# Optimization experiments

Hardware: AMD Instinct MI355X
Metric: run time of the kernel (lower is better)

## Reference

```python
import jax, jax.numpy as jnp
import numpy as np

B = 131072
K = 1024
D = 16 * 8  # hard-coded feature dim in the torch module


def setup_inputs() -> dict:
    key = jax.random.key(0)
    kx, kw = jax.random.split(key)
    x = jax.random.normal(kx, (B, D), dtype=jnp.float32)
    # xavier_normal_ init: std = sqrt(2 / (fan_in + fan_out)) = sqrt(2 / (K + D))
    std = np.sqrt(2.0 / (K + D)).astype(np.float32)
    cluster_weights = jax.random.normal(kw, (K, D), dtype=jnp.float32) * std
    return {"x": x, "cluster_weights": cluster_weights}


def reference(x, cluster_weights):
    bn = x.shape[0]
    k = cluster_weights.shape[0]
    x = x.reshape(bn, -1)  # [B, D]
    # (same math as the original broadcasted (x - w)^2 sum, without the [B,K,D] blow-up)
    x2 = jnp.sum(x * x, axis=1, keepdims=True)               # [B, 1]
    w2 = jnp.sum(cluster_weights * cluster_weights, axis=1)  # [K]
    d = x2 + w2[None, :] - 2.0 * jnp.matmul(x, cluster_weights.T)  # [B, K]
    cl = jnp.argmin(d, axis=1)  # [B] int
    # distance to assigned centroid, summed
    inertia_loss = jnp.sum(jnp.take_along_axis(d, cl[:, None], axis=1))
    # xe_loss = sum_{i,j} (1 if i==j else -1) * <w_i, w_j>
    #         = 2 * trace(W W^T) - sum(W W^T)
    G = jnp.matmul(cluster_weights, cluster_weights.T)  # [K, K]
    xe_loss = 2.0 * jnp.trace(G) - jnp.sum(G)
    return inertia_loss / bn, xe_loss / k, cl
```

## Files before the change

### kernel.cpp

```cpp
#include <hip/hip_runtime.h>
#include <float.h>
#include <limits.h>
#include <math.h>


#define TAU 1e-3f

using bf16x8 = __attribute__((ext_vector_type(8))) short;
using f32x4  = __attribute__((ext_vector_type(4))) float;
using s16x4  = __attribute__((ext_vector_type(4))) short;

static __device__ __forceinline__ short f2bf_trunc(float f) {
    return (short)(__float_as_uint(f) >> 16);
}
static __device__ __forceinline__ float bf2f(short h) {
    return __uint_as_float(((unsigned int)(unsigned short)h) << 16);
}
static __device__ __forceinline__ bool lexlt(float v1, int i1, float v2, int i2) {
    return v1 < v2 || (v1 == v2 && i1 < i2);
}
static __device__ __forceinline__ void gload_lds16(const void* g, void* l) {
    __builtin_amdgcn_global_load_lds(
        (const __attribute__((address_space(1))) unsigned int*)g,
        (__attribute__((address_space(3))) unsigned int*)l, 16, 0, 0);
}
#define FENCE() do { asm volatile("" ::: "memory"); __builtin_amdgcn_sched_barrier(0); } while (0)

__global__ void wprep_kernel(const float* __restrict__ W, float* __restrict__ w2,
                             short* __restrict__ whl, int write_whl)
{
    const int k = blockIdx.x;
    const int d = threadIdx.x;
    float v = W[(size_t)k * 128 + d];
    float sq = v * v;
    for (int off = 1; off < 64; off <<= 1) sq += __shfl_xor(sq, off, 64);
    __shared__ float p[2];
    if ((d & 63) == 0) p[d >> 6] = sq;
    __syncthreads();
    if (d == 0) w2[k] = p[0] + p[1];
    if (write_whl) {
        short h = f2bf_trunc(v);
        short l = f2bf_trunc(v - bf2f(h));
        const int tile = k >> 7, c = k & 127;
        size_t base = (size_t)tile * 32768 + (size_t)(c >> 4) * 2048 + (size_t)(d >> 5) * 512
                    + (size_t)((d >> 3) & 3) * 128 + (size_t)(c & 15) * 8 + (size_t)(d & 7);
        whl[base]         = h;
        whl[base + 16384] = l;
    }
}

__global__ __launch_bounds__(512, 1)
void dist_argmin_mfma(const float* __restrict__ X, const short* __restrict__ whl,
                      const float* __restrict__ w2g, float* __restrict__ cl_out,
                      double* __restrict__ inertia_acc,
                      int* __restrict__ flag_cnt, int* __restrict__ flag_rows,
                      int flag_cap)
{
    __shared__ __align__(16) char smem[137856];
    char*   lB0  = smem;
    char*   lB1  = smem + 65536;
    float*  lw2  = (float*)(smem + 131072);
    float*  lx2  = (float*)(smem + 135168);
    int*    mscr = (int*)(smem + 135680);
    double* dred = (double*)(smem + 137728);

    const int tid    = threadIdx.x;
    const int lane   = tid & 63;
    const int laneLo = lane & 15;
    const int laneHi = lane >> 4;
    const int wid    = tid >> 6;
    const int rowg   = wid >> 1;
    const int colg   = wid & 1;
    const int rowbase = blockIdx.x * 128;

    lw2[tid]       = w2g[tid];
    lw2[tid + 512] = w2g[tid + 512];

    {
        const int r = tid >> 2, q = tid & 3;
        float s = 0.f;
        short* Areg = (short*)lB0;
        #pragma unroll
        for (int j = 0; j < 8; ++j) {
            const int d0 = q * 4 + j * 16;
            float4 v = *reinterpret_cast<const float4*>(X + (size_t)(rowbase + r) * 128 + d0);
            float fv[4] = {v.x, v.y, v.z, v.w};
            s16x4 hv, lv;
            #pragma unroll
            for (int u = 0; u < 4; ++u) {
                s = fmaf(fv[u], fv[u], s);
                short h = f2bf_trunc(fv[u]);
                short l = f2bf_trunc(fv[u] - bf2f(h));
                hv[u] = h; lv[u] = l;
            }
            const int kb = d0 >> 3, off = d0 & 7;
            short* pa = Areg + ((size_t)kb * 128 + r) * 8 + off;
            *reinterpret_cast<s16x4*>(pa)         = hv;
            *reinterpret_cast<s16x4*>(pa + 16384) = lv;
        }
        s += __shfl_xor(s, 1, 64);
        s += __shfl_xor(s, 2, 64);
        if (q == 0) lx2[r] = s;
    }
    __syncthreads();

    bf16x8 ah[2][4], al[2][4];
    {
        const char* pA = lB0 + laneHi * 2048 + (rowg * 32 + laneLo) * 16;
        #pragma unroll
        for (int k0b = 0; k0b < 4; ++k0b)
            #pragma unroll
            for (int m = 0; m < 2; ++m) {
                ah[m][k0b] = *reinterpret_cast<const bf16x8*>(pA + k0b * 8192 + m * 256);
                al[m][k0b] = *reinterpret_cast<const bf16x8*>(pA + 32768 + k0b * 8192 + m * 256);
            }
    }
    asm volatile("s_waitcnt lgkmcnt(0)" ::: "memory");
    __builtin_amdgcn_sched_barrier(0);
    __builtin_amdgcn_s_barrier();
    FENCE();

    #pragma unroll
    for (int q = 0; q < 8; ++q)
        gload_lds16((const char*)whl + (q * 8 + wid) * 1024 + lane * 16,
                    lB0 + (q * 8 + wid) * 1024);

    float t1v[2][4], t2v[2][4];
    int   t1i[2][4];
    #pragma unroll
    for (int m = 0; m < 2; ++m)
        #pragma unroll
        for (int r = 0; r < 4; ++r) {
            t1v[m][r] = FLT_MAX; t2v[m][r] = FLT_MAX; t1i[m][r] = INT_MAX;
        }
    int colv[4];
    #pragma unroll
    for (int nt = 0; nt < 4; ++nt) colv[nt] = colg * 64 + nt * 16 + laneLo;

    const char* pB0 = lB0 + colg * 16384 + lane * 16;
    const char* pB1 = lB1 + colg * 16384 + lane * 16;

    auto compute = [&](int t, const char* pB) {
        float w2v[4];
        #pragma unroll
        for (int nt = 0; nt < 4; ++nt)
            w2v[nt] = lw2[t * 128 + colg * 64 + nt * 16 + laneLo];

        f32x4 acc[2][4];
        #pragma unroll
        for (int m = 0; m < 2; ++m)
            #pragma unroll
            for (int nt = 0; nt < 4; ++nt)
                acc[m][nt] = (f32x4){0.f, 0.f, 0.f, 0.f};

        __builtin_amdgcn_s_setprio(1);
        #pragma unroll
        for (int k0b = 0; k0b < 4; ++k0b) {
            #pragma unroll
            for (int nt = 0; nt < 4; ++nt) {
                bf16x8 bh = *reinterpret_cast<const bf16x8*>(pB + nt * 4096 + k0b * 1024);
                bf16x8 bl = *reinterpret_cast<const bf16x8*>(pB + 32768 + nt * 4096 + k0b * 1024);
                #pragma unroll
                for (int m = 0; m < 2; ++m) {
                    acc[m][nt] = __builtin_amdgcn_mfma_f32_16x16x32_bf16(ah[m][k0b], bh, acc[m][nt], 0, 0, 0);
                    acc[m][nt] = __builtin_amdgcn_mfma_f32_16x16x32_bf16(ah[m][k0b], bl, acc[m][nt], 0, 0, 0);
                    acc[m][nt] = __builtin_amdgcn_mfma_f32_16x16x32_bf16(al[m][k0b], bh, acc[m][nt], 0, 0, 0);
                }
            }
        }
        __builtin_amdgcn_s_setprio(0);

        #pragma unroll
        for (int nt = 0; nt < 4; ++nt)
            #pragma unroll
            for (int m = 0; m < 2; ++m)
                #pragma unroll
                for (int r = 0; r < 4; ++r) {
                    float dv = fmaf(-2.f, acc[m][nt][r], w2v[nt]);
                    float hi = fmaxf(t1v[m][r], dv);
                    t2v[m][r] = fminf(t2v[m][r], hi);
                    bool cnd = dv < t1v[m][r];
                    t1i[m][r] = cnd ? colv[nt] : t1i[m][r];
                    t1v[m][r] = fminf(t1v[m][r], dv);
                }
        #pragma unroll
        for (int nt = 0; nt < 4; ++nt) colv[nt] += 128;
    };

    #pragma unroll 2
    for (int t = 0; t < 7; ++t) {
        char* dst = ((t + 1) & 1) ? lB1 : lB0;
        const char* src = (const char*)whl + (size_t)(t + 1) * 65536;
        #pragma unroll
        for (int q = 0; q < 8; ++q)
            gload_lds16(src + (q * 8 + wid) * 1024 + lane * 16,
                        dst + (q * 8 + wid) * 1024);
        asm volatile("s_waitcnt vmcnt(8)" ::: "memory");
        __builtin_amdgcn_sched_barrier(0);
        __builtin_amdgcn_s_barrier();
        FENCE();
        compute(t, (t & 1) ? pB1 : pB0);
        asm volatile("s_waitcnt lgkmcnt(0)" ::: "memory");
        __builtin_amdgcn_sched_barrier(0);
        __builtin_amdgcn_s_barrier();
        FENCE();
    }
    asm volatile("s_waitcnt vmcnt(0)" ::: "memory");
    __builtin_amdgcn_sched_barrier(0);
    __builtin_amdgcn_s_barrier();
    FENCE();
    compute(7, pB1);

    #pragma unroll
    for (int off = 1; off < 16; off <<= 1) {
        #pragma unroll
        for (int m = 0; m < 2; ++m)
            #pragma unroll
            for (int r = 0; r < 4; ++r) {
                float ov1 = __shfl_xor(t1v[m][r], off, 64);
                int   oi1 = __shfl_xor(t1i[m][r], off, 64);
                float ov2 = __shfl_xor(t2v[m][r], off, 64);
                float nt2 = fminf(fminf(t2v[m][r], ov2), fmaxf(t1v[m][r], ov1));
                if (lexlt(ov1, oi1, t1v[m][r], t1i[m][r])) { t1v[m][r] = ov1; t1i[m][r] = oi1; }
                t2v[m][r] = nt2;
            }
    }

    __syncthreads();
    if (colg == 1 && laneLo == 0) {
        #pragma unroll
        for (int m = 0; m < 2; ++m)
            #pragma unroll
            for (int r = 0; r < 4; ++r) {
                const int row = rowg * 32 + m * 16 + laneHi * 4 + r;
                mscr[row * 4 + 0] = __float_as_int(t1v[m][r]);
                mscr[row * 4 + 1] = t1i[m][r];
                mscr[row * 4 + 2] = __float_as_int(t2v[m][r]);
            }
    }
    __syncthreads();
    double local = 0.0;
    if (colg == 0 && laneLo == 0) {
        #pragma unroll
        for (int m = 0; m < 2; ++m)
            #pragma unroll
            for (int r = 0; r < 4; ++r) {
                const int row = rowg * 32 + m * 16 + laneHi * 4 + r;
                float ov1 = __int_as_float(mscr[row * 4 + 0]);
                int   oi1 = mscr[row * 4 + 1];
                float ov2 = __int_as_float(mscr[row * 4 + 2]);
                float b1v = t1v[m][r], b2v;
                int   b1i = t1i[m][r];
                b2v = fminf(fminf(t2v[m][r], ov2), fmaxf(b1v, ov1));
                if (lexlt(ov1, oi1, b1v, b1i)) { b1v = ov1; b1i = oi1; }
                const int grow = rowbase + row;
                const float gap = b2v - b1v;
                if (gap >= TAU) {
                    cl_out[grow] = (float)b1i;
                    local += (double)(b1v + lx2[row]);
                } else {
                    int slot = atomicAdd(flag_cnt, 1);
                    if (slot < flag_cap) {
                        flag_rows[slot] = grow;
                    } else {
                        cl_out[grow] = (float)b1i;
                        local += (double)(b1v + lx2[row]);
                    }
                }
            }
        dred[rowg * 4 + laneHi] = local;
    }
    __syncthreads();
    if (tid == 0) {
        double tt = 0.0;
        for (int i = 0; i < 16; ++i) tt += dred[i];
        atomicAdd(inertia_acc, tt);
    }
}

__global__ __launch_bounds__(512, 1)
void dist_argmin_v2(const float* __restrict__ X, const float* __restrict__ W,
                    const float* __restrict__ w2g, float* __restrict__ cl_out,
                    double* __restrict__ inertia_acc,
                    int* __restrict__ flag_cnt, int* __restrict__ flag_rows,
                    int flag_cap)
{
    __shared__ __align__(16) char smem[133760];
    short*  Areg = (short*)smem;
    short*  Breg = (short*)(smem + 65536);
    int*    mscr = (int*)(smem + 131072);
    float*  lx2  = (float*)(smem + 131072 + 2048);
    double* dred = (double*)(smem + 131072 + 2048 + 512);

    const int tid    = threadIdx.x;
    const int lane   = tid & 63;
    const int laneLo = lane & 15;
    const int laneHi = lane >> 4;
    const int wid    = tid >> 6;
    const int rowg   = wid >> 1;
    const int colg   = wid & 1;
    const int rowbase = blockIdx.x * 128;

    {
        const int r = tid >> 2, q = tid & 3;
        float s = 0.f;
        #pragma unroll
        for (int j = 0; j < 8; ++j) {
            const int d0 = q * 4 + j * 16;
            float4 v = *reinterpret_cast<const float4*>(X + (size_t)(rowbase + r) * 128 + d0);
            float fv[4] = {v.x, v.y, v.z, v.w};
            s16x4 hv, lv;
            #pragma unroll
            for (int u = 0; u < 4; ++u) {
                s = fmaf(fv[u], fv[u], s);
                short h = f2bf_trunc(fv[u]);
                short l = f2bf_trunc(fv[u] - bf2f(h));
                hv[u] = h; lv[u] = l;
            }
            const int kb = d0 >> 3, off = d0 & 7;
            short* pa = Areg + (kb * 128 + r) * 8 + off;
            *reinterpret_cast<s16x4*>(pa)         = hv;
            *reinterpret_cast<s16x4*>(pa + 16384) = lv;
        }
        s += __shfl_xor(s, 1, 64);
        s += __shfl_xor(s, 2, 64);
        if (q == 0) lx2[r] = s;
    }

    float t1v[2][4], t2v[2][4];
    int   t1i[2][4];
    #pragma unroll
    for (int m = 0; m < 2; ++m)
        #pragma unroll
        for (int r = 0; r < 4; ++r) {
            t1v[m][r] = FLT_MAX; t2v[m][r] = FLT_MAX; t1i[m][r] = INT_MAX;
        }

    const char* pAbase = smem + laneHi * 2048 + (rowg * 32 + laneLo) * 16;
    const char* pBbase = smem + 65536 + colg * 16384 + lane * 16;

    for (int iter = 0; iter < 8; ++iter) {
        __syncthreads();
        {
            const int c = tid >> 2, q = tid & 3;
            const int nt = c >> 4, c15 = c & 15;
            #pragma unroll
            for (int j = 0; j < 8; ++j) {
                const int d0 = q * 4 + j * 16;
                float4 v = *reinterpret_cast<const float4*>(W + (size_t)(iter * 128 + c) * 128 + d0);
                float fv[4] = {v.x, v.y, v.z, v.w};
                s16x4 hv, lv;
                #pragma unroll
                for (int u = 0; u < 4; ++u) {
                    short h = f2bf_trunc(fv[u]);
                    short l = f2bf_trunc(fv[u] - bf2f(h));
                    hv[u] = h; lv[u] = l;
                }
                const int k0b = d0 >> 5, sub = (d0 >> 3) & 3, jj = d0 & 7;
                short* pb = Breg + ((nt * 4 + k0b) * 64 + sub * 16 + c15) * 8 + jj;
                *reinterpret_cast<s16x4*>(pb)         = hv;
                *reinterpret_cast<s16x4*>(pb + 16384) = lv;
            }
        }
        float w2v[4];
        #pragma unroll
        for (int nt = 0; nt < 4; ++nt)
            w2v[nt] = w2g[iter * 128 + colg * 64 + nt * 16 + laneLo];
        __syncthreads();

        f32x4 acc[2][4];
        #pragma unroll
        for (int m = 0; m < 2; ++m)
            #pragma unroll
            for (int nt = 0; nt < 4; ++nt)
                acc[m][nt] = (f32x4){0.f, 0.f, 0.f, 0.f};

        #pragma unroll
        for (int k0b = 0; k0b < 4; ++k0b) {
            bf16x8 ah[2], al[2];
            #pragma unroll
            for (int m = 0; m < 2; ++m) {
                ah[m] = *reinterpret_cast<const bf16x8*>(pAbase + k0b * 8192 + m * 256);
                al[m] = *reinterpret_cast<const bf16x8*>(pAbase + 32768 + k0b * 8192 + m * 256);
            }
            #pragma unroll
            for (int nt = 0; nt < 4; ++nt) {
                bf16x8 bh = *reinterpret_cast<const bf16x8*>(pBbase + nt * 4096 + k0b * 1024);
                bf16x8 bl = *reinterpret_cast<const bf16x8*>(pBbase + 32768 + nt * 4096 + k0b * 1024);
                #pragma unroll
                for (int m = 0; m < 2; ++m) {
                    acc[m][nt] = __builtin_amdgcn_mfma_f32_16x16x32_bf16(ah[m], bh, acc[m][nt], 0, 0, 0);
                    acc[m][nt] = __builtin_amdgcn_mfma_f32_16x16x32_bf16(ah[m], bl, acc[m][nt], 0, 0, 0);
                    acc[m][nt] = __builtin_amdgcn_mfma_f32_16x16x32_bf16(al[m], bh, acc[m][nt], 0, 0, 0);
                }
            }
        }

        #pragma unroll
        for (int nt = 0; nt < 4; ++nt) {
            const int col = iter * 128 + colg * 64 + nt * 16 + laneLo;
            #pragma unroll
            for (int m = 0; m < 2; ++m)
                #pragma unroll
                for (int r = 0; r < 4; ++r) {
                    float dv = fmaf(-2.f, acc[m][nt][r], w2v[nt]);
                    float hi = fmaxf(t1v[m][r], dv);
                    t2v[m][r] = fminf(t2v[m][r], hi);
                    bool cnd = dv < t1v[m][r];
                    t1i[m][r] = cnd ? col : t1i[m][r];
                    t1v[m][r] = fminf(t1v[m][r], dv);
                }
        }
    }

    #pragma unroll
    for (int off = 1; off < 16; off <<= 1) {
        #pragma unroll
        for (int m = 0; m < 2; ++m)
            #pragma unroll
            for (int r = 0; r < 4; ++r) {
                float ov1 = __shfl_xor(t1v[m][r], off, 64);
                int   oi1 = __shfl_xor(t1i[m][r], off, 64);
                float ov2 = __shfl_xor(t2v[m][r], off, 64);
                float nt2 = fminf(fminf(t2v[m][r], ov2), fmaxf(t1v[m][r], ov1));
                if (lexlt(ov1, oi1, t1v[m][r], t1i[m][r])) { t1v[m][r] = ov1; t1i[m][r] = oi1; }
                t2v[m][r] = nt2;
            }
    }

    __syncthreads();
    if (colg == 1 && laneLo == 0) {
        #pragma unroll
        for (int m = 0; m < 2; ++m)
            #pragma unroll
            for (int r = 0; r < 4; ++r) {
                const int row = rowg * 32 + m * 16 + laneHi * 4 + r;
                mscr[row * 4 + 0] = __float_as_int(t1v[m][r]);
                mscr[row * 4 + 1] = t1i[m][r];
                mscr[row * 4 + 2] = __float_as_int(t2v[m][r]);
            }
    }
    __syncthreads();
    double local = 0.0;
    if (colg == 0 && laneLo == 0) {
        #pragma unroll
        for (int m = 0; m < 2; ++m)
            #pragma unroll
            for (int r = 0; r < 4; ++r) {
                const int row = rowg * 32 + m * 16 + laneHi * 4 + r;
                float ov1 = __int_as_float(mscr[row * 4 + 0]);
                int   oi1 = mscr[row * 4 + 1];
                float ov2 = __int_as_float(mscr[row * 4 + 2]);
                float b1v = t1v[m][r], b2v;
                int   b1i = t1i[m][r];
                b2v = fminf(fminf(t2v[m][r], ov2), fmaxf(b1v, ov1));
                if (lexlt(ov1, oi1, b1v, b1i)) { b1v = ov1; b1i = oi1; }
                const int grow = rowbase + row;
                const float gap = b2v - b1v;
                if (gap >= TAU) {
                    cl_out[grow] = (float)b1i;
                    local += (double)(b1v + lx2[row]);
                } else {
                    int slot = atomicAdd(flag_cnt, 1);
                    if (slot < flag_cap) flag_rows[slot] = grow;
                    else { cl_out[grow] = (float)b1i; local += (double)(b1v + lx2[row]); }
                }
            }
        dred[rowg * 4 + laneHi] = local;
    }
    __syncthreads();
    if (tid == 0) {
        double t = 0.0;
        for (int i = 0; i < 16; ++i) t += dred[i];
        atomicAdd(inertia_acc, t);
    }
}

__global__ void refine_kernel(const float* __restrict__ X, const float* __restrict__ W,
                              const int* __restrict__ flag_cnt, const int* __restrict__ flag_rows,
                              int flag_cap, float* __restrict__ cl_out,
                              double* __restrict__ inertia_acc)
{
    __shared__ double sv[4];
    __shared__ int    si[4];
    __shared__ float  xrow[128];
    int n = *flag_cnt;
    if (n > flag_cap) n = flag_cap;
    const int tid = threadIdx.x;

    for (int f = blockIdx.x; f < n; f += gridDim.x) {
        int row = flag_rows[f];
        if (tid < 128) xrow[tid] = X[(size_t)row * 128 + tid];
        __syncthreads();

        double best = DBL_MAX; int bi = INT_MAX;
        for (int cc = 0; cc < 4; ++cc) {
            int c = tid + 256 * cc;
            double dot = 0.0, wsq = 0.0;
            for (int d = 0; d < 128; ++d) {
                double wv = (double)W[(size_t)c * 128 + d];
                dot = fma((double)xrow[d], wv, dot);
                wsq = fma(wv, wv, wsq);
            }
            double dist = wsq - 2.0 * dot;
            if (dist < best || (dist == best && c < bi)) { best = dist; bi = c; }
        }
        for (int off = 1; off < 64; off <<= 1) {
            double ov = __shfl_xor(best, off, 64);
            int    oi = __shfl_xor(bi, off, 64);
            if (ov < best || (ov == best && oi < bi)) { best = ov; bi = oi; }
        }
        if ((tid & 63) == 0) { sv[tid >> 6] = best; si[tid >> 6] = bi; }
        __syncthreads();
        if (tid == 0) {
            for (int wv = 1; wv < 4; ++wv)
                if (sv[wv] < best || (sv[wv] == best && si[wv] < bi)) { best = sv[wv]; bi = si[wv]; }
            double x2 = 0.0;
            for (int d = 0; d < 128; ++d) { double xv = (double)xrow[d]; x2 = fma(xv, xv, x2); }
            cl_out[row] = (float)bi;
            atomicAdd(inertia_acc, x2 + best);
        }
        __syncthreads();
    }
}

__global__ void finalize_kernel(const float* __restrict__ W, const float* __restrict__ w2,
                                const double* __restrict__ inertia, float* __restrict__ out)
{
    __shared__ float sh1[128], sh2[128];
    int d = threadIdx.x;
    float s = 0.f;
    for (int k = 0; k < 1024; ++k) s += W[(size_t)k * 128 + d];
    float t = 0.f;
    for (int j = 0; j < 8; ++j) t += w2[d + 128 * j];
    sh1[d] = s * s;
    sh2[d] = t;
    __syncthreads();
    for (int off = 64; off > 0; off >>= 1) {
        if (d < off) { sh1[d] += sh1[d + off]; sh2[d] += sh2[d + off]; }
        __syncthreads();
    }
    if (d == 0) {
        float xe = 2.f * sh2[0] - sh1[0];
        out[1] = xe / 1024.f;
        out[0] = (float)(*inertia / 131072.0);
    }
}

extern "C" void kernel_launch(void* const* d_in, const int* in_sizes, int n_in,
                              void* d_out, int out_size, void* d_ws, size_t ws_size,
                              hipStream_t stream)
{
    const float* X = (const float*)d_in[0];
    const float* W = (const float*)d_in[1];
    float* out = (float*)d_out;
    char* ws = (char*)d_ws;

    double* inertia  = (double*)ws;
    int*    flag_cnt = (int*)(ws + 8);
    float*  w2       = (float*)(ws + 16);
    short*  whl      = (short*)(ws + 8192);

    const size_t WHL_END = 8192 + 524288;
    const bool precomp = ws_size >= WHL_END + 65536;

    int*   flag_rows;
    int    flag_cap;
    if (precomp) {
        flag_rows = (int*)(ws + WHL_END);
        long cap = ((long)ws_size - (long)WHL_END) / 4;
        flag_cap = cap > 131072 ? 131072 : (int)cap;
    } else {
        flag_rows = (int*)(ws + 8192);
        long cap = ((long)ws_size - 8192) / 4;
        flag_cap = cap < 0 ? 0 : (cap > 131072 ? 131072 : (int)cap);
    }

    hipMemsetAsync(ws, 0, 16, stream);

    wprep_kernel<<<1024, 128, 0, stream>>>(W, w2, whl, precomp ? 1 : 0);
    if (precomp) {
        dist_argmin_mfma<<<1024, 512, 0, stream>>>(X, whl, w2, out + 2, inertia,
                                                   flag_cnt, flag_rows, flag_cap);
    } else {
        dist_argmin_v2<<<1024, 512, 0, stream>>>(X, W, w2, out + 2, inertia,
                                                 flag_cnt, flag_rows, flag_cap);
    }
    refine_kernel<<<1024, 256, 0, stream>>>(X, W, flag_cnt, flag_rows, flag_cap,
                                            out + 2, inertia);
    finalize_kernel<<<1, 128, 0, stream>>>(W, w2, inertia, out);
}
```

Baseline: 202.3 us.

## Halve centroid tile to 64 columns and load X directly into registers

The centroid tile streamed through LDS shrinks from 128 to 64 columns, so the double buffer and shared memory drop to roughly half. Launch bounds now allow several 512-thread blocks per CU. X rows are converted to bf16 hi/lo fragments straight from global memory into registers, which removes the LDS staging pass and one block barrier. The compute loop is reordered per column tile to lower accumulator register pressure, at the cost of more, smaller pipeline iterations and more barriers per block.

```diff
diff --git a/kernel.cpp b/kernel.cpp
--- a/kernel.cpp
+++ b/kernel.cpp
@@ -41,28 +41,28 @@
     if (write_whl) {
         short h = f2bf_trunc(v);
         short l = f2bf_trunc(v - bf2f(h));
-        const int tile = k >> 7, c = k & 127;
-        size_t base = (size_t)tile * 32768 + (size_t)(c >> 4) * 2048 + (size_t)(d >> 5) * 512
+        const int tile = k >> 6, c = k & 63;
+        size_t base = (size_t)tile * 16384 + (size_t)(c >> 4) * 2048 + (size_t)(d >> 5) * 512
                     + (size_t)((d >> 3) & 3) * 128 + (size_t)(c & 15) * 8 + (size_t)(d & 7);
-        whl[base]         = h;
-        whl[base + 16384] = l;
-    }
-}
-
-__global__ __launch_bounds__(512, 1)
+        whl[base]        = h;
+        whl[base + 8192] = l;
+    }
+}
+
+__global__ __launch_bounds__(512, 4)
 void dist_argmin_mfma(const float* __restrict__ X, const short* __restrict__ whl,
                       const float* __restrict__ w2g, float* __restrict__ cl_out,
                       double* __restrict__ inertia_acc,
                       int* __restrict__ flag_cnt, int* __restrict__ flag_rows,
                       int flag_cap)
 {
-    __shared__ __align__(16) char smem[137856];
+    __shared__ __align__(16) char smem[72320];
     char*   lB0  = smem;
-    char*   lB1  = smem + 65536;
-    float*  lw2  = (float*)(smem + 131072);
-    float*  lx2  = (float*)(smem + 135168);
-    int*    mscr = (int*)(smem + 135680);
-    double* dred = (double*)(smem + 137728);
+    char*   lB1  = smem + 32768;
+    float*  lw2  = (float*)(smem + 65536);
+    float*  lx2  = (float*)(smem + 69632);
+    int*    mscr = (int*)(smem + 70144);
+    double* dred = (double*)(smem + 72192);
 
     const int tid    = threadIdx.x;
     const int lane   = tid & 63;
@@ -76,54 +76,39 @@
     lw2[tid]       = w2g[tid];
     lw2[tid + 512] = w2g[tid + 512];
 
-    {
-        const int r = tid >> 2, q = tid & 3;
+    bf16x8 ah[2][4], al[2][4];
+    #pragma unroll
+    for (int m = 0; m < 2; ++m) {
+        const float* xp = X + (size_t)(rowbase + rowg * 32 + m * 16 + laneLo) * 128 + laneHi * 8;
         float s = 0.f;
-        short* Areg = (short*)lB0;
-        #pragma unroll
-        for (int j = 0; j < 8; ++j) {
-            const int d0 = q * 4 + j * 16;
-            float4 v = *reinterpret_cast<const float4*>(X + (size_t)(rowbase + r) * 128 + d0);
-            float fv[4] = {v.x, v.y, v.z, v.w};
-            s16x4 hv, lv;
-            #pragma unroll
-            for (int u = 0; u < 4; ++u) {
+        #pragma unroll
+        for (int k0b = 0; k0b < 4; ++k0b) {
+            float4 v0 = *reinterpret_cast<const float4*>(xp + k0b * 32);
+            float4 v1 = *reinterpret_cast<const float4*>(xp + k0b * 32 + 4);
+            float fv[8] = {v0.x, v0.y, v0.z, v0.w, v1.x, v1.y, v1.z, v1.w};
+            bf16x8 hv, lv;
+            #pragma unroll
+            for (int u = 0; u < 8; ++u) {
                 s = fmaf(fv[u], fv[u], s);
                 short h = f2bf_trunc(fv[u]);
                 short l = f2bf_trunc(fv[u] - bf2f(h));
                 hv[u] = h; lv[u] = l;
             }
-            const int kb = d0 >> 3, off = d0 & 7;
-            short* pa = Areg + ((size_t)kb * 128 + r) * 8 + off;
-            *reinterpret_cast<s16x4*>(pa)         = hv;
-            *reinterpret_cast<s16x4*>(pa + 16384) = lv;
-        }
-        s += __shfl_xor(s, 1, 64);
-        s += __shfl_xor(s, 2, 64);
-        if (q == 0) lx2[r] = s;
-    }
-    __syncthreads();
-
-    bf16x8 ah[2][4], al[2][4];
-    {
-        const char* pA = lB0 + laneHi * 2048 + (rowg * 32 + laneLo) * 16;
-        #pragma unroll
-        for (int k0b = 0; k0b < 4; ++k0b)
-            #pragma unroll
-            for (int m = 0; m < 2; ++m) {
-                ah[m][k0b] = *reinterpret_cast<const bf16x8*>(pA + k0b * 8192 + m * 256);
-                al[m][k0b] = *reinterpret_cast<const bf16x8*>(pA + 32768 + k0b * 8192 + m * 256);
-            }
+            ah[m][k0b] = hv; al[m][k0b] = lv;
+        }
+        s += __shfl_xor(s, 16, 64);
+        s += __shfl_xor(s, 32, 64);
+        if (colg == 0 && laneHi == 0) lx2[rowg * 32 + m * 16 + laneLo] = s;
     }
     asm volatile("s_waitcnt lgkmcnt(0)" ::: "memory");
     __builtin_amdgcn_sched_barrier(0);
-    __builtin_amdgcn_s_barrier();
-    FENCE();
-
+
+    const char* wsrc = (const char*)whl;
     #pragma unroll
-    for (int q = 0; q < 8; ++q)
-        gload_lds16((const char*)whl + (q * 8 + wid) * 1024 + lane * 16,
-                    lB0 + (q * 8 + wid) * 1024);
+    for (int q = 0; q < 4; ++q)
+        gload_lds16(wsrc + wid * 4096 + q * 1024 + lane * 16,
+                    lB0 + wid * 4096 + q * 1024);
+    wsrc += 32768;
 
     float t1v[2][4], t2v[2][4];
     int   t1i[2][4];
@@ -133,83 +118,71 @@
         for (int r = 0; r < 4; ++r) {
             t1v[m][r] = FLT_MAX; t2v[m][r] = FLT_MAX; t1i[m][r] = INT_MAX;
         }
-    int colv[4];
-    #pragma unroll
-    for (int nt = 0; nt < 4; ++nt) colv[nt] = colg * 64 + nt * 16 + laneLo;
-
-    const char* pB0 = lB0 + colg * 16384 + lane * 16;
-    const char* pB1 = lB1 + colg * 16384 + lane * 16;
-
-    auto compute = [&](int t, const char* pB) {
-        float w2v[4];
-        #pragma unroll
-        for (int nt = 0; nt < 4; ++nt)
-            w2v[nt] = lw2[t * 128 + colg * 64 + nt * 16 + laneLo];
-
-        f32x4 acc[2][4];
-        #pragma unroll
-        for (int m = 0; m < 2; ++m)
-            #pragma unroll
-            for (int nt = 0; nt < 4; ++nt)
-                acc[m][nt] = (f32x4){0.f, 0.f, 0.f, 0.f};
-
+
+    const float* w2p = lw2 + colg * 32 + laneLo;
+    int colbase = colg * 32 + laneLo;
+
+    auto compute = [&](const char* pB) {
+        const char* pBb = pB + colg * 8192 + lane * 16;
         __builtin_amdgcn_s_setprio(1);
         #pragma unroll
-        for (int k0b = 0; k0b < 4; ++k0b) {
-            #pragma unroll
-            for (int nt = 0; nt < 4; ++nt) {
-                bf16x8 bh = *reinterpret_cast<const bf16x8*>(pB + nt * 4096 + k0b * 1024);
-                bf16x8 bl = *reinterpret_cast<const bf16x8*>(pB + 32768 + nt * 4096 + k0b * 1024);
-                #pragma unroll
-                for (int m = 0; m < 2; ++m) {
-                    acc[m][nt] = __builtin_amdgcn_mfma_f32_16x16x32_bf16(ah[m][k0b], bh, acc[m][nt], 0, 0, 0);
-                    acc[m][nt] = __builtin_amdgcn_mfma_f32_16x16x32_bf16(ah[m][k0b], bl, acc[m][nt], 0, 0, 0);
-                    acc[m][nt] = __builtin_amdgcn_mfma_f32_16x16x32_bf16(al[m][k0b], bh, acc[m][nt], 0, 0, 0);
-                }
+        for (int nt = 0; nt < 2; ++nt) {
+            float w2v = w2p[nt * 16];
+            f32x4 a0 = (f32x4){0.f, 0.f, 0.f, 0.f};
+            f32x4 a1 = (f32x4){0.f, 0.f, 0.f, 0.f};
+            #pragma unroll
+            for (int k0b = 0; k0b < 4; ++k0b) {
+                bf16x8 bh = *reinterpret_cast<const bf16x8*>(pBb + nt * 4096 + k0b * 1024);
+                bf16x8 bl = *reinterpret_cast<const bf16x8*>(pBb + 16384 + nt * 4096 + k0b * 1024);
+                a0 = __builtin_amdgcn_mfma_f32_16x16x32_bf16(ah[0][k0b], bh, a0, 0, 0, 0);
+                a0 = __builtin_amdgcn_mfma_f32_16x16x32_bf16(ah[0][k0b], bl, a0, 0, 0, 0);
+                a0 = __builtin_amdgcn_mfma_f32_16x16x32_bf16(al[0][k0b], bh, a0, 0, 0, 0);
+                a1 = __builtin_amdgcn_mfma_f32_16x16x32_bf16(ah[1][k0b], bh, a1, 0, 0, 0);
+                a1 = __builtin_amdgcn_mfma_f32_16x16x32_bf16(ah[1][k0b], bl, a1, 0, 0, 0);
+                a1 = __builtin_amdgcn_mfma_f32_16x16x32_bf16(al[1][k0b], bh, a1, 0, 0, 0);
+            }
+            const int col = colbase + nt * 16;
+            #pragma unroll
+            for (int r = 0; r < 4; ++r) {
+                float dv0 = fmaf(-2.f, a0[r], w2v);
+                t2v[0][r] = fminf(t2v[0][r], fmaxf(t1v[0][r], dv0));
+                t1i[0][r] = (dv0 < t1v[0][r]) ? col : t1i[0][r];
+                t1v[0][r] = fminf(t1v[0][r], dv0);
+                float dv1 = fmaf(-2.f, a1[r], w2v);
+                t2v[1][r] = fminf(t2v[1][r], fmaxf(t1v[1][r], dv1));
+                t1i[1][r] = (dv1 < t1v[1][r]) ? col : t1i[1][r];
+                t1v[1][r] = fminf(t1v[1][r], dv1);
             }
         }
         __builtin_amdgcn_s_setprio(0);
-
-        #pragma unroll
-        for (int nt = 0; nt < 4; ++nt)
-            #pragma unroll
-            for (int m = 0; m < 2; ++m)
-                #pragma unroll
-                for (int r = 0; r < 4; ++r) {
-                    float dv = fmaf(-2.f, acc[m][nt][r], w2v[nt]);
-                    float hi = fmaxf(t1v[m][r], dv);
-                    t2v[m][r] = fminf(t2v[m][r], hi);
-                    bool cnd = dv < t1v[m][r];
-                    t1i[m][r] = cnd ? colv[nt] : t1i[m][r];
-                    t1v[m][r] = fminf(t1v[m][r], dv);
-                }
-        #pragma unroll
-        for (int nt = 0; nt < 4; ++nt) colv[nt] += 128;
     };
 
-    #pragma unroll 2
-    for (int t = 0; t < 7; ++t) {
-        char* dst = ((t + 1) & 1) ? lB1 : lB0;
-        const char* src = (const char*)whl + (size_t)(t + 1) * 65536;
-        #pragma unroll
-        for (int q = 0; q < 8; ++q)
-            gload_lds16(src + (q * 8 + wid) * 1024 + lane * 16,
-                        dst + (q * 8 + wid) * 1024);
-        asm volatile("s_waitcnt vmcnt(8)" ::: "memory");
+    const char* cur = lB0;
+    char*       nxt = lB1;
+    #pragma unroll 1
+    for (int t = 0; t < 15; ++t) {
+        #pragma unroll
+        for (int q = 0; q < 4; ++q)
+            gload_lds16(wsrc + wid * 4096 + q * 1024 + lane * 16,
+                        nxt + wid * 4096 + q * 1024);
+        wsrc += 32768;
+        asm volatile("s_waitcnt vmcnt(4)" ::: "memory");
         __builtin_amdgcn_sched_barrier(0);
         __builtin_amdgcn_s_barrier();
         FENCE();
-        compute(t, (t & 1) ? pB1 : pB0);
+        compute(cur);
+        w2p += 64; colbase += 64;
         asm volatile("s_waitcnt lgkmcnt(0)" ::: "memory");
         __builtin_amdgcn_sched_barrier(0);
         __builtin_amdgcn_s_barrier();
         FENCE();
+        char* tmp = nxt; nxt = (char*)cur; cur = tmp;
     }
     asm volatile("s_waitcnt vmcnt(0)" ::: "memory");
     __builtin_amdgcn_sched_barrier(0);
     __builtin_amdgcn_s_barrier();
     FENCE();
-    compute(7, pB1);
+    compute(cur);
 
     #pragma unroll
     for (int off = 1; off < 16; off <<= 1) {
```

New measurement: 171.0 us. 1.18x faster.
